# Optimization experiments

Hardware: AMD Instinct MI355X
Metric: run time of the kernel (lower is better)

Reference implementation:

```python
import jax, jax.numpy as jnp
import numpy as np


def setup_inputs() -> dict:
    key = jax.random.key(0)
    k1, k2 = jax.random.split(key)
    B, C, H, W = 8, 64, 128, 256
    left_feature = jax.random.normal(k1, (B, C, H, W), dtype=jnp.float32)
    right_feature = jax.random.normal(k2, (B, C, H, W), dtype=jnp.float32)
    return {
        "left_feature": left_feature,
        "right_feature": right_feature,
        "max_disp": 64,
    }


def reference(left_feature, right_feature, max_disp):
    # Stereo correlation cost volume (norm=False branch):
    #   volume[b, d, h, w] = mean_c( left[b,c,h,w] * right[b,c,h,w-d] )  for w >= d
    #   volume[b, d, h, w] = 0                                           for w <  d
    b, c, h, w = left_feature.shape

    def corr_at_disp(d):
        # left[:, :, :, d:] * right[:, :, :, :w-d], mean over channel dim
        prod = left_feature[:, :, :, d:] * right_feature[:, :, :, : w - d]
        cv = jnp.mean(prod, axis=1)  # (b, h, w-d)
        # left-pad along width with zeros for invalid disparities
        return jnp.pad(cv, ((0, 0), (0, 0), (d, 0)))

    # max_disp is a static Python int; loop over disparity hyperparameter is static.
    volume = jnp.stack([corr_at_disp(d) for d in range(max_disp)], axis=1)
    return volume  # (b, max_disp, h, w)
```

## Files before the change

### kernel.cpp

```cpp
#include <hip/hip_runtime.h>

typedef _Float16 half8 __attribute__((ext_vector_type(8)));
typedef float floatx4 __attribute__((ext_vector_type(4)));

#define BB 8
#define CC 64
#define HH 128
#define WW 256
#define DD 64
#define NROW 4
#define GRID 256
#define OPITCH 260

#define BAR() asm volatile("s_waitcnt lgkmcnt(0)\n\ts_barrier" ::: "memory")

__global__ __launch_bounds__(512, 2)
void corr_volume_mfma(const float* __restrict__ left,
                      const float* __restrict__ right,
                      float* __restrict__ out) {
    __shared__ alignas(16) unsigned char smem[73728];
    _Float16* const Lb = (_Float16*)smem;
    _Float16* const Rb = (_Float16*)(smem + 32768);
    float*    const Ob = (float*)smem;

    const int tid  = threadIdx.x;
    const int lane = tid & 63;
    const int wv   = tid >> 6;
    const int sw   = lane * 4;
    const int cg   = wv;

    const size_t chanStride = (size_t)HH * WW;

    float4 lv[8], rv[8];

    {
        const int bh = blockIdx.x;
        const size_t rowBase = (size_t)(bh >> 7) * CC * chanStride
                             + (size_t)(bh & 127) * WW;
        const float* lp = left  + rowBase + (size_t)(cg * 8) * chanStride + sw;
        const float* rp = right + rowBase + (size_t)(cg * 8) * chanStride + sw;
        #pragma unroll
        for (int c = 0; c < 8; ++c) {
            lv[c] = *(const float4*)(lp + (size_t)c * chanStride);
            rv[c] = *(const float4*)(rp + (size_t)c * chanStride);
        }
    }

    const int n = lane & 15;
    const int q = lane >> 4;
    const int wbase = wv * 32;
    const float scale = 1.0f / 64.0f;

    #pragma unroll
    for (int k = 0; k < NROW; ++k) {
        const int bh = blockIdx.x + k * GRID;
        const int b  = bh >> 7;
        const int h  = bh & 127;

        BAR();

        {
            half8 z = {0, 0, 0, 0, 0, 0, 0, 0};
            *(half8*)&Rb[tid * 8] = z;
        }

        {
            const float* lf = (const float*)lv;
            const float* rf = (const float*)rv;
            #pragma unroll
            for (int s = 0; s < 4; ++s) {
                const int w   = sw + s;
                const int col = (cg ^ (w & 7)) * 8;
                half8 lh, rh;
                #pragma unroll
                for (int c = 0; c < 8; ++c) {
                    lh[c] = (_Float16)lf[c * 4 + s];
                    rh[c] = (_Float16)rf[c * 4 + s];
                }
                *(half8*)&Lb[w * 64 + col]        = lh;
                *(half8*)&Rb[(w + 64) * 64 + col] = rh;
            }
        }

        const float* lp2 = nullptr;
        const float* rp2 = nullptr;
        if (k + 1 < NROW) {
            const int bh2 = blockIdx.x + (k + 1) * GRID;
            const size_t rowBase2 = (size_t)(bh2 >> 7) * CC * chanStride
                                  + (size_t)(bh2 & 127) * WW;
            lp2 = left  + rowBase2 + (size_t)(cg * 8) * chanStride + sw;
            rp2 = right + rowBase2 + (size_t)(cg * 8) * chanStride + sw;
            #pragma unroll
            for (int c = 0; c < 4; ++c)
                lv[c] = *(const float4*)(lp2 + (size_t)c * chanStride);
        }

        BAR();

        if (k + 1 < NROW) {
            #pragma unroll
            for (int c = 4; c < 8; ++c)
                lv[c] = *(const float4*)(lp2 + (size_t)c * chanStride);
        }

        floatx4 acc[2][5];
        #pragma unroll
        for (int t = 0; t < 2; ++t)
            #pragma unroll
            for (int u = 0; u < 5; ++u)
                #pragma unroll
                for (int r = 0; r < 4; ++r)
                    acc[t][u][r] = 0.0f;

        #pragma unroll
        for (int kk = 0; kk < 2; ++kk) {
            const int col = ((kk * 4 + q) ^ (n & 7)) * 8;
            half8 bfrag[2], afrag[6];
            #pragma unroll
            for (int t = 0; t < 2; ++t)
                bfrag[t] = *(const half8*)&Lb[(wbase + t * 16 + n) * 64 + col];
            #pragma unroll
            for (int a = 0; a < 6; ++a)
                afrag[a] = *(const half8*)&Rb[(wbase + a * 16 + n) * 64 + col];
            #pragma unroll
            for (int t = 0; t < 2; ++t)
                #pragma unroll
                for (int u = 0; u < 5; ++u)
                    acc[t][u] = __builtin_amdgcn_mfma_f32_16x16x32_f16(
                        afrag[t + u], bfrag[t], acc[t][u], 0, 0, 0);

            if (kk == 0 && k + 1 < NROW) {
                #pragma unroll
                for (int c = 0; c < 4; ++c)
                    rv[c] = *(const float4*)(rp2 + (size_t)c * chanStride);
            }
        }
        BAR();

        if (k + 1 < NROW) {
            #pragma unroll
            for (int c = 4; c < 8; ++c)
                rv[c] = *(const float4*)(rp2 + (size_t)c * chanStride);
        }

        #pragma unroll
        for (int t = 0; t < 2; ++t) {
            const int w = wbase + t * 16 + n;
            #pragma unroll
            for (int u = 0; u < 5; ++u) {
                #pragma unroll
                for (int r = 0; r < 4; ++r) {
                    const int d = 64 - 16 * u + n - (q * 4 + r);
                    if (d >= 0 && d < DD) {
                        Ob[d * OPITCH + w] = acc[t][u][r] * scale;
                    }
                }
            }
        }
        BAR();

        #pragma unroll
        for (int i = 0; i < 8; ++i) {
            const int d = wv * 8 + i;
            const floatx4 v = *(const floatx4*)&Ob[d * OPITCH + lane * 4];
            floatx4* dst = (floatx4*)&out[(((size_t)b * DD + d) * HH + h) * WW + lane * 4];
            __builtin_nontemporal_store(v, dst);
        }
    }
}

extern "C" void kernel_launch(void* const* d_in, const int* in_sizes, int n_in,
                              void* d_out, int out_size, void* d_ws, size_t ws_size,
                              hipStream_t stream) {
    const float* left  = (const float*)d_in[0];
    const float* right = (const float*)d_in[1];
    float* out = (float*)d_out;

    dim3 grid(GRID);
    dim3 block(512);
    corr_volume_mfma<<<grid, block, 0, stream>>>(left, right, out);
}
```

Baseline: 171.7 us.

## Split each block's work across two rows by width halves with right-feature halo

Each block now handles two image rows, h and h^64. Half the threads compute output widths 0-127 of one row and the other half compute widths 128-255 of the other row. The second half loads an extra 64-column halo of right features so it has every disparity it needs, and the output store phase writes 128-wide half-row segments. The intent is to change the global access and store pattern, and to spread rows across blocks differently. In exchange it adds redundant halo reads and a little more LDS per block (81920 bytes, which still fits two blocks per CU).

```diff
diff --git a/kernel.cpp b/kernel.cpp
--- a/kernel.cpp
+++ b/kernel.cpp
@@ -1,6 +1,7 @@
 #include <hip/hip_runtime.h>
 
 typedef _Float16 half8 __attribute__((ext_vector_type(8)));
+typedef _Float16 half4_t __attribute__((ext_vector_type(4)));
 typedef float floatx4 __attribute__((ext_vector_type(4)));
 
 #define BB 8
@@ -18,7 +19,7 @@
 void corr_volume_mfma(const float* __restrict__ left,
                       const float* __restrict__ right,
                       float* __restrict__ out) {
-    __shared__ alignas(16) unsigned char smem[73728];
+    __shared__ alignas(16) unsigned char smem[81920];
     _Float16* const Lb = (_Float16*)smem;
     _Float16* const Rb = (_Float16*)(smem + 32768);
     float*    const Ob = (float*)smem;
@@ -26,36 +27,54 @@
     const int tid  = threadIdx.x;
     const int lane = tid & 63;
     const int wv   = tid >> 6;
-    const int sw   = lane * 4;
-    const int cg   = wv;
+
+    const int hf  = tid >> 8;
+    const int st  = tid & 255;
+    const int cg  = st >> 5;
+    const int wq  = (st & 31) * 4;
+    const int cg4 = st >> 4;
+    const int wq4 = (st & 15) * 4;
 
     const size_t chanStride = (size_t)HH * WW;
 
-    float4 lv[8], rv[8];
+    const int hA = blockIdx.x & 127;
+    const int hB = hA ^ 64;
+    const int hS = hf ? hB : hA;
+    const int W0 = hf << 7;
+
+    float4 lv[8], rv[8], rx[4];
 
     {
-        const int bh = blockIdx.x;
-        const size_t rowBase = (size_t)(bh >> 7) * CC * chanStride
-                             + (size_t)(bh & 127) * WW;
-        const float* lp = left  + rowBase + (size_t)(cg * 8) * chanStride + sw;
-        const float* rp = right + rowBase + (size_t)(cg * 8) * chanStride + sw;
+        const int b0 = blockIdx.x >> 7;
+        const size_t rowBase = (size_t)b0 * CC * chanStride + (size_t)hS * WW;
+        const float* lp = left  + rowBase + (size_t)(cg * 8) * chanStride + W0 + wq;
+        const float* rp = right + rowBase + (size_t)(cg * 8) * chanStride + W0 + wq;
         #pragma unroll
         for (int c = 0; c < 8; ++c) {
             lv[c] = *(const float4*)(lp + (size_t)c * chanStride);
             rv[c] = *(const float4*)(rp + (size_t)c * chanStride);
         }
+        if (hf) {
+            const float* rq = right + rowBase + (size_t)(cg4 * 4) * chanStride + 64 + wq4;
+            #pragma unroll
+            for (int c = 0; c < 4; ++c)
+                rx[c] = *(const float4*)(rq + (size_t)c * chanStride);
+        }
     }
 
-    const int n = lane & 15;
-    const int q = lane >> 4;
-    const int wbase = wv * 32;
+    const int n   = lane & 15;
+    const int q   = lane >> 4;
+    const int hfw = wv >> 2;
+    const int wb  = (wv & 3) * 32;
+    _Float16* const Lh = Lb + hfw * (128 * 64);
+    _Float16* const Rh = Rb + hfw * (192 * 64);
+    const int hOut = hfw ? hB : hA;
+    const int W0w  = hfw << 7;
     const float scale = 1.0f / 64.0f;
 
     #pragma unroll
     for (int k = 0; k < NROW; ++k) {
-        const int bh = blockIdx.x + k * GRID;
-        const int b  = bh >> 7;
-        const int h  = bh & 127;
+        const int b = (blockIdx.x >> 7) + 2 * k;
 
         BAR();
 
@@ -69,27 +88,40 @@
             const float* rf = (const float*)rv;
             #pragma unroll
             for (int s = 0; s < 4; ++s) {
-                const int w   = sw + s;
-                const int col = (cg ^ (w & 7)) * 8;
+                const int wl   = wq + s;
+                const int colL = (cg ^ (wl & 7)) * 8;
+                const int j    = 64 + wl;
+                const int colR = (cg ^ (j & 7)) * 8;
                 half8 lh, rh;
                 #pragma unroll
                 for (int c = 0; c < 8; ++c) {
                     lh[c] = (_Float16)lf[c * 4 + s];
                     rh[c] = (_Float16)rf[c * 4 + s];
                 }
-                *(half8*)&Lb[w * 64 + col]        = lh;
-                *(half8*)&Rb[(w + 64) * 64 + col] = rh;
-            }
-        }
-
-        const float* lp2 = nullptr;
-        const float* rp2 = nullptr;
+                *(half8*)&Lb[hf * 8192  + wl * 64 + colL] = lh;
+                *(half8*)&Rb[hf * 12288 + j  * 64 + colR] = rh;
+            }
+            if (hf) {
+                const float* rg = (const float*)rx;
+                #pragma unroll
+                for (int s = 0; s < 4; ++s) {
+                    const int j  = wq4 + s;
+                    const int cb = ((cg4 >> 1) ^ (j & 7)) * 8 + (cg4 & 1) * 4;
+                    half4_t v;
+                    #pragma unroll
+                    for (int c = 0; c < 4; ++c) v[c] = (_Float16)rg[c * 4 + s];
+                    *(half4_t*)&Rb[12288 + j * 64 + cb] = v;
+                }
+            }
+        }
+
+        const float *lp2 = nullptr, *rp2 = nullptr, *rq2 = nullptr;
         if (k + 1 < NROW) {
-            const int bh2 = blockIdx.x + (k + 1) * GRID;
-            const size_t rowBase2 = (size_t)(bh2 >> 7) * CC * chanStride
-                                  + (size_t)(bh2 & 127) * WW;
-            lp2 = left  + rowBase2 + (size_t)(cg * 8) * chanStride + sw;
-            rp2 = right + rowBase2 + (size_t)(cg * 8) * chanStride + sw;
+            const int b2 = (blockIdx.x >> 7) + 2 * (k + 1);
+            const size_t rowBase2 = (size_t)b2 * CC * chanStride + (size_t)hS * WW;
+            lp2 = left  + rowBase2 + (size_t)(cg * 8) * chanStride + W0 + wq;
+            rp2 = right + rowBase2 + (size_t)(cg * 8) * chanStride + W0 + wq;
+            rq2 = right + rowBase2 + (size_t)(cg4 * 4) * chanStride + 64 + wq4;
             #pragma unroll
             for (int c = 0; c < 4; ++c)
                 lv[c] = *(const float4*)(lp2 + (size_t)c * chanStride);
@@ -118,10 +150,10 @@
             half8 bfrag[2], afrag[6];
             #pragma unroll
             for (int t = 0; t < 2; ++t)
-                bfrag[t] = *(const half8*)&Lb[(wbase + t * 16 + n) * 64 + col];
+                bfrag[t] = *(const half8*)&Lh[(wb + t * 16 + n) * 64 + col];
             #pragma unroll
             for (int a = 0; a < 6; ++a)
-                afrag[a] = *(const half8*)&Rb[(wbase + a * 16 + n) * 64 + col];
+                afrag[a] = *(const half8*)&Rh[(wb + a * 16 + n) * 64 + col];
             #pragma unroll
             for (int t = 0; t < 2; ++t)
                 #pragma unroll
@@ -141,11 +173,16 @@
             #pragma unroll
             for (int c = 4; c < 8; ++c)
                 rv[c] = *(const float4*)(rp2 + (size_t)c * chanStride);
+            if (hf) {
+                #pragma unroll
+                for (int c = 0; c < 4; ++c)
+                    rx[c] = *(const float4*)(rq2 + (size_t)c * chanStride);
+            }
         }
 
         #pragma unroll
         for (int t = 0; t < 2; ++t) {
-            const int w = wbase + t * 16 + n;
+            const int w = W0w + wb + t * 16 + n;
             #pragma unroll
             for (int u = 0; u < 5; ++u) {
                 #pragma unroll
@@ -161,9 +198,10 @@
 
         #pragma unroll
         for (int i = 0; i < 8; ++i) {
-            const int d = wv * 8 + i;
-            const floatx4 v = *(const floatx4*)&Ob[d * OPITCH + lane * 4];
-            floatx4* dst = (floatx4*)&out[(((size_t)b * DD + d) * HH + h) * WW + lane * 4];
+            const int d = (wv & 3) * 16 + i * 2 + (lane >> 5);
+            const int w = W0w + (lane & 31) * 4;
+            const floatx4 v = *(const floatx4*)&Ob[d * OPITCH + w];
+            floatx4* dst = (floatx4*)&out[(((size_t)b * DD + d) * HH + hOut) * WW + w];
             __builtin_nontemporal_store(v, dst);
         }
     }
```

Result: no change. 171.5 us (-0.1%).
